# Performance work log

Hardware: AMD Instinct MI355X
Metric: run time of the kernel (lower is better)

Reference implementation:

```python
import jax, jax.numpy as jnp
import numpy as np

B, L, K, E, H, NH, W_OFF = 8, 512, 16, 32, 1, 64, 1
DK = E // H


def setup_inputs() -> dict:
    key = jax.random.key(0)
    ks = jax.random.split(key, 12)
    return {
        "time_steps": jax.random.uniform(ks[0], (B, L), jnp.float32),
        "val": jax.random.normal(ks[1], (B, L), jnp.float32),
        "mark": jax.random.randint(ks[2], (B, L), 1, K + 1, dtype=jnp.int32),
        "non_pad_mask": jnp.ones((B, L, 1), jnp.float32),
        "Wl": jax.random.normal(ks[3], (1, 1), jnp.float32) * 0.5,
        "bl": jnp.zeros((1,), jnp.float32),
        "Wp": jax.random.normal(ks[4], (E - 1, 1), jnp.float32) * 0.5,
        "bp": jnp.zeros((E - 1,), jnp.float32),
        "Wq": jax.random.normal(ks[5], (E, E), jnp.float32) / np.sqrt(E).astype(np.float32),
        "bq": jnp.zeros((E,), jnp.float32),
        "Wk": jax.random.normal(ks[6], (E, E), jnp.float32) / np.sqrt(E).astype(np.float32),
        "bk": jnp.zeros((E,), jnp.float32),
        "Wo": jax.random.normal(ks[7], (NH, K * H), jnp.float32) / np.sqrt(K * H).astype(np.float32),
        "bo": jnp.zeros((NH,), jnp.float32),
        "W_ih": jax.random.normal(ks[8], (3 * NH, NH), jnp.float32) / np.sqrt(NH).astype(np.float32),
        "W_hh": jax.random.normal(ks[9], (3 * NH, NH), jnp.float32) / np.sqrt(NH).astype(np.float32),
        "b_ih": jnp.zeros((3 * NH,), jnp.float32),
        "b_hh": jnp.zeros((3 * NH,), jnp.float32),
    }


def _forward(time_steps, val, mark, non_pad_mask,
             Wl, bl, Wp, bp, Wq, bq, Wk, bk, Wo, bo,
             W_ih, W_hh, b_ih, b_hh):
    # transform_to_3d_ts: scatter each (b,l) event into its channel mark-1
    npm = non_pad_mask[:, :, 0]                       # [B,L]
    onehot = (mark - 1)[:, :, None] == jnp.arange(K)[None, None, :]  # [B,L,K]
    valid = onehot & (npm > 0)[:, :, None]
    val_blk = jnp.where(valid, val[:, :, None], 0.0)          # [B,L,K]
    mask_blk = jnp.where(valid, npm[:, :, None], 0.0)         # [B,L,K]

    # learn_time_embedding
    tt = time_steps[:, :, None]                                # [B,L,1]
    key_emb = jnp.concatenate([tt @ Wl.T + bl, jnp.sin(tt @ Wp.T + bp)], axis=-1)  # [B,L,E]

    # subsequent mask (tril with diag offset w)
    att_mask = jnp.tril(jnp.ones((L, L), jnp.float32), W_OFF)  # [L,L]

    # multiTimeAttention (query == key == key_emb)
    q = (key_emb @ Wq.T + bq).reshape(B, L, H, DK).transpose(0, 2, 1, 3)  # [B,H,L,DK]
    k = (key_emb @ Wk.T + bk).reshape(B, L, H, DK).transpose(0, 2, 1, 3)
    scores = jnp.einsum('bhqd,bhkd->bhqk', q, k) / jnp.sqrt(jnp.float32(DK))  # [B,H,L,L]
    # broadcast to [B,H,L,L,K] (repeat_interleave equivalent), apply att_mask then pad mask
    scores5 = scores[..., None] * att_mask[None, None, :, :, None]
    scores5 = jnp.where(mask_blk[:, None, None, :, :] == 0, -1e9, scores5)
    p_attn = jax.nn.softmax(scores5, axis=-2)                  # softmax over key positions
    x = jnp.sum(p_attn * val_blk[:, None, None, :, :], axis=-2)  # [B,H,L,K]
    x = x.transpose(0, 2, 1, 3).reshape(B, L, H * K)
    att_out = x @ Wo.T + bo                                    # [B,L,NH]

    # single-layer GRU over time (PyTorch gate equations)
    def step(h, xt):
        gi = xt @ W_ih.T + b_ih
        gh = h @ W_hh.T + b_hh
        ir, iz, inn = jnp.split(gi, 3, axis=-1)
        hr, hz, hn = jnp.split(gh, 3, axis=-1)
        r = jax.nn.sigmoid(ir + hr)
        z = jax.nn.sigmoid(iz + hz)
        n = jnp.tanh(inn + r * hn)
        h_new = (1.0 - z) * n + z * h
        return h_new, h_new

    h0 = jnp.zeros((B, NH), att_out.dtype)
    _, outs = jax.lax.scan(step, h0, att_out.transpose(1, 0, 2))  # [L,B,NH]
    return outs.transpose(1, 0, 2)                                # [B,L,NH]


def reference(time_steps, val, mark, non_pad_mask,
              Wl, bl, Wp, bp, Wq, bq, Wk, bk, Wo, bo,
              W_ih, W_hh, b_ih, b_hh):
    return _forward(time_steps, val, mark, non_pad_mask,
                    Wl, bl, Wp, bp, Wq, bq, Wk, bk, Wo, bo,
                    W_ih, W_hh, b_ih, b_hh)
```

## Files before the change

kernel.cpp:

```cpp
#include <hip/hip_runtime.h>
#include <math.h>

#define B_    8
#define L_    512
#define K_    16
#define E_    32
#define NH_   64
#define WOFF_ 1


typedef float v2f __attribute__((ext_vector_type(2)));
typedef float v4f __attribute__((ext_vector_type(4)));

__global__ __launch_bounds__(256) void k_fused(
    const float* __restrict__ ts,   const float* __restrict__ val,
    const int*   __restrict__ mark, const float* __restrict__ npm,
    const float* __restrict__ Wl,   const float* __restrict__ bl,
    const float* __restrict__ Wp,   const float* __restrict__ bp,
    const float* __restrict__ Wq,   const float* __restrict__ bq,
    const float* __restrict__ Wk,   const float* __restrict__ bk,
    const float* __restrict__ Wo,   const float* __restrict__ bo,
    const float* __restrict__ Wih,  const float* __restrict__ bih,
    float* __restrict__ gi)
{
    __shared__ float kL[32 * 512];
    __shared__ float qL[16 * 32];
    __shared__ float srow[4 * 512];
    __shared__ int   cc[512];
    __shared__ float vv[512];
    __shared__ float attL[16 * 64];
    __shared__ float WqL[1024], WkL[1024];
    __shared__ float bqL[32], bkL[32], WpL[31], bpL[31];
    __shared__ float wl0, bl0;

    const int tid = threadIdx.x;
    const int qb  = blockIdx.x;
    const int b   = blockIdx.y;
    const int qb0 = qb * 16;

    {
        float4 v = ((const float4*)Wq)[tid];
        ((float4*)WqL)[tid] = v;
        float4 u = ((const float4*)Wk)[tid];
        ((float4*)WkL)[tid] = u;
    }
    if (tid < 32) { bqL[tid] = bq[tid]; bkL[tid] = bk[tid]; }
    if (tid < 31) { WpL[tid] = Wp[tid]; bpL[tid] = bp[tid]; }
    if (tid == 0) { wl0 = Wl[0]; bl0 = bl[0]; }
    for (int k = tid; k < 512; k += 256) {
        const int   m  = mark[b * 512 + k];
        const float np = npm[b * 512 + k];
        cc[k] = (np > 0.0f) ? (m - 1) : -1;
        vv[k] = val[b * 512 + k];
    }
    __syncthreads();

    for (int l = tid; l < 512; l += 256) {
        const float t = ts[b * 512 + l];
        float e[32];
        e[0] = t * wl0 + bl0;
        #pragma unroll
        for (int j = 1; j < 32; ++j) e[j] = sinf(t * WpL[j - 1] + bpL[j - 1]);

        const bool ownq = (l >= qb0) && (l < qb0 + 16);
        float* qrow = qL + (l - qb0) * 32;

        for (int dq = 0; dq < 8; ++dq) {
            float k0 = bkL[4*dq+0], k1 = bkL[4*dq+1], k2 = bkL[4*dq+2], k3 = bkL[4*dq+3];
            const float* wk = &WkL[(4*dq) * 32];
            #pragma unroll
            for (int j = 0; j < 32; ++j) {
                const float ej = e[j];
                k0 = fmaf(wk[j],      ej, k0);
                k1 = fmaf(wk[32 + j], ej, k1);
                k2 = fmaf(wk[64 + j], ej, k2);
                k3 = fmaf(wk[96 + j], ej, k3);
            }
            kL[(4*dq + 0) * 512 + l] = k0;
            kL[(4*dq + 1) * 512 + l] = k1;
            kL[(4*dq + 2) * 512 + l] = k2;
            kL[(4*dq + 3) * 512 + l] = k3;

            if (ownq) {
                float q0 = bqL[4*dq+0], q1 = bqL[4*dq+1], q2 = bqL[4*dq+2], q3 = bqL[4*dq+3];
                const float* wq = &WqL[(4*dq) * 32];
                #pragma unroll
                for (int j = 0; j < 32; ++j) {
                    const float ej = e[j];
                    q0 = fmaf(wq[j],      ej, q0);
                    q1 = fmaf(wq[32 + j], ej, q1);
                    q2 = fmaf(wq[64 + j], ej, q2);
                    q3 = fmaf(wq[96 + j], ej, q3);
                }
                qrow[4*dq + 0] = q0;
                qrow[4*dq + 1] = q1;
                qrow[4*dq + 2] = q2;
                qrow[4*dq + 3] = q3;
            }
        }
    }
    __syncthreads();

    const int w = tid >> 6, lane = tid & 63;

    for (int iq = 0; iq < 4; ++iq) {
        const int q = qb0 + w * 4 + iq;

        float qr[32];
        const float4* qm4 = (const float4*)(qL + (size_t)(q - qb0) * 32);
        #pragma unroll
        for (int j4 = 0; j4 < 8; ++j4) {
            float4 v = qm4[j4];
            qr[4*j4+0] = v.x; qr[4*j4+1] = v.y; qr[4*j4+2] = v.z; qr[4*j4+3] = v.w;
        }

        float acc[8];
        #pragma unroll
        for (int m = 0; m < 8; ++m) acc[m] = 0.0f;
        #pragma unroll 4
        for (int j = 0; j < 32; ++j) {
            const float* row = kL + j * 512 + lane;
            const float  qj  = qr[j];
            #pragma unroll
            for (int m = 0; m < 8; ++m) acc[m] = fmaf(qj, row[m * 64], acc[m]);
        }
        #pragma unroll
        for (int m = 0; m < 8; ++m)
            srow[w * 512 + m * 64 + lane] = acc[m] * 0.17677669529663687f;
        __syncthreads();

        const int c = lane & 15, s = lane >> 4;
        float mx = -1e30f, Z = 0.0f, X = 0.0f;
        const int base = s * 128;
        for (int t = 0; t < 128; ++t) {
            const int k = base + ((t + s) & 127);
            if (cc[k] == c) {
                const float l  = (k <= q + WOFF_) ? srow[w * 512 + k] : 0.0f;
                const float mn = fmaxf(mx, l);
                const float e1 = __expf(l - mn);
                const float sc = __expf(mx - mn);
                Z = Z * sc + e1;
                X = X * sc + e1 * vv[k];
                mx = mn;
            }
        }
        #pragma unroll
        for (int off = 16; off <= 32; off <<= 1) {
            const float mo = __shfl_xor(mx, off);
            const float Zo = __shfl_xor(Z, off);
            const float Xo = __shfl_xor(X, off);
            const float mn = fmaxf(mx, mo);
            const float a0 = __expf(mx - mn);
            const float a1 = __expf(mo - mn);
            Z = Z * a0 + Zo * a1;
            X = X * a0 + Xo * a1;
            mx = mn;
        }
        const float x = (Z > 0.0f) ? X / Z : 0.0f;

        float xs[16];
        #pragma unroll
        for (int c2 = 0; c2 < 16; ++c2) xs[c2] = __shfl(x, c2);

        const float4* wo4 = (const float4*)(Wo + lane * 16);
        float a = bo[lane];
        #pragma unroll
        for (int c4 = 0; c4 < 4; ++c4) {
            float4 v = wo4[c4];
            a += xs[4*c4+0] * v.x + xs[4*c4+1] * v.y + xs[4*c4+2] * v.z + xs[4*c4+3] * v.w;
        }
        attL[(w * 4 + iq) * 64 + lane] = a;
        __syncthreads();
    }

    const size_t out0 = (size_t)(b * 32 + qb) * 16 * 192;
    for (int pp = 0; pp < 12; ++pp) {
        const int p = tid + 256 * pp;
        const int r = p / 192, g = p - r * 192;
        float a0 = bih[g], a1 = 0.f, a2 = 0.f, a3 = 0.f;
        const float* wrow = Wih + g * 64;
        const float* arow = &attL[r * 64];
        #pragma unroll
        for (int j = 0; j < 64; j += 4) {
            a0 = fmaf(arow[j + 0], wrow[j + 0], a0);
            a1 = fmaf(arow[j + 1], wrow[j + 1], a1);
            a2 = fmaf(arow[j + 2], wrow[j + 2], a2);
            a3 = fmaf(arow[j + 3], wrow[j + 3], a3);
        }
        gi[out0 + p] = (a0 + a1) + (a2 + a3);
    }
}


#define GRU_STEP(u, DO_REFILL) {                                           \
    v4f hv[16];                                                            \
                                       \
    _Pragma("unroll")                                                      \
    for (int k = 0; k < 6; ++k) hv[k] = hs4[k];                            \
    const float gr = pr[u], gz = pz[u], gn = pn[u];                        \
    if (DO_REFILL) {                                                       \
        pr[u] = pf[0];                                                     \
        pz[u] = pf[64];                                                    \
        pn[u] = pf[128];                                                   \
        pf += 192;                                                         \
    }                                                                      \
    v2f ar2 = {gr + br, 0.0f};                                             \
    v2f az2 = {gz + bz, 0.0f};                                             \
    v2f an2 = {bn, 0.0f};                                                  \
    _Pragma("unroll")                                                      \
    for (int k = 0; k < 16; ++k) {                                         \
        if (k < 10) hv[k + 6] = hs4[k + 6];              \
        v2f p0 = __builtin_shufflevector(hv[k], hv[k], 0, 1);              \
        v2f p1 = __builtin_shufflevector(hv[k], hv[k], 2, 3);              \
        ar2 = wr[2*k]     * p0 + ar2;                    \
        az2 = wz[2*k]     * p0 + az2;                                      \
        an2 = wn[2*k]     * p0 + an2;                                      \
        ar2 = wr[2*k + 1] * p1 + ar2;                                      \
        az2 = wz[2*k + 1] * p1 + az2;                                      \
        an2 = wn[2*k + 1] * p1 + an2;                                      \
    }                                                                      \
    const float ar = ar2.x + ar2.y;                                        \
    const float az = az2.x + az2.y;                                        \
    const float hn = an2.x + an2.y;                                        \
    const float r = __builtin_amdgcn_rcpf(1.0f + __expf(-ar));             \
    const float z = __builtin_amdgcn_rcpf(1.0f + __expf(-az));             \
    float npre = gn + r * hn;                                              \
    npre = fminf(fmaxf(npre, -15.0f), 15.0f);                              \
    const float e2 = __expf(2.0f * npre);                                  \
    const float n  = (e2 - 1.0f) * __builtin_amdgcn_rcpf(e2 + 1.0f);       \
    h = fmaf(z, h - n, n);                              \
    hs[lane] = h;                        \
    *outp = h;                                        \
    outp += 64;                                                            \
}

__global__ __launch_bounds__(64, 1) void k_gru(
    const float* __restrict__ gi, const float* __restrict__ Whh,
    const float* __restrict__ bhh, float* __restrict__ out)
{
    __shared__ float hs[64];
    const int lane = threadIdx.x;
    const int b    = blockIdx.x;

    v2f wr[32], wz[32], wn[32];
    {
        const v2f* r2 = (const v2f*)(Whh + (size_t)lane * 64);
        const v2f* z2 = (const v2f*)(Whh + (size_t)(lane + 64) * 64);
        const v2f* n2 = (const v2f*)(Whh + (size_t)(lane + 128) * 64);
        #pragma unroll
        for (int j = 0; j < 32; ++j) {
            wr[j] = r2[j];
            wz[j] = z2[j];
            wn[j] = n2[j];
        }
    }
    const float br = bhh[lane];
    const float bz = bhh[lane + 64];
    const float bn = bhh[lane + 128];

    const float* gib  = gi  + (size_t)b * 512 * 192;
    float*       outp = out + (size_t)b * 512 * 64 + lane;

    float h = 0.0f;
    hs[lane] = 0.0f;

    float pr[2], pz[2], pn[2];
    #pragma unroll
    for (int i = 0; i < 2; ++i) {
        const float* gp = gib + (size_t)i * 192;
        pr[i] = gp[lane];
        pz[i] = gp[lane + 64];
        pn[i] = gp[lane + 128];
    }
    const float* pf = gib + (size_t)2 * 192 + lane;

    const v4f* hs4 = (const v4f*)hs;

    for (int tt = 0; tt < 510; tt += 2) {
        GRU_STEP(0, 1)
        GRU_STEP(1, 1)
    }
    GRU_STEP(0, 0)
    GRU_STEP(1, 0)
}

extern "C" void kernel_launch(void* const* d_in, const int* in_sizes, int n_in,
                              void* d_out, int out_size, void* d_ws, size_t ws_size,
                              hipStream_t stream)
{
    const float* ts   = (const float*)d_in[0];
    const float* val  = (const float*)d_in[1];
    const int*   mark = (const int*)  d_in[2];
    const float* npm  = (const float*)d_in[3];
    const float* Wl   = (const float*)d_in[4];
    const float* bl   = (const float*)d_in[5];
    const float* Wp   = (const float*)d_in[6];
    const float* bp   = (const float*)d_in[7];
    const float* Wq   = (const float*)d_in[8];
    const float* bq   = (const float*)d_in[9];
    const float* Wk   = (const float*)d_in[10];
    const float* bk   = (const float*)d_in[11];
    const float* Wo   = (const float*)d_in[12];
    const float* bo   = (const float*)d_in[13];
    const float* Wih  = (const float*)d_in[14];
    const float* Whh  = (const float*)d_in[15];
    const float* bih  = (const float*)d_in[16];
    const float* bhh  = (const float*)d_in[17];

    float* ws    = (float*)d_ws;
    float* gi    = ws + 524288;
    float* out   = (float*)d_out;

    k_fused<<<dim3(32, 8), 256, 0, stream>>>(ts, val, mark, npm, Wl, bl, Wp, bp,
                                             Wq, bq, Wk, bk, Wo, bo, Wih, bih, gi);
    k_gru<<<8, 64, 0, stream>>>(gi, Whh, bhh, out);
}
```

Measured before the change: 384.5 us.

## Fuse attention and GRU kernels with per-chunk flags to overlap the recurrence

Merges the attention/input-projection kernel and the GRU recurrence into one launch. The first 8 blocks run the GRU and spin on per-(batch, chunk) flags, and the remaining 256 blocks compute gi chunks and release a flag when each chunk is done. The GRU can then start on early time chunks while later ones are still being computed, hiding most of the attention phase and removing the second launch. It depends on all blocks being co-resident to avoid deadlock, and it adds a memset plus spin-waiting overhead.

```diff
diff --git a/kernel.cpp b/kernel.cpp
--- a/kernel.cpp
+++ b/kernel.cpp
@@ -12,7 +12,54 @@
 typedef float v2f __attribute__((ext_vector_type(2)));
 typedef float v4f __attribute__((ext_vector_type(4)));
 
-__global__ __launch_bounds__(256) void k_fused(
+
+#define GRU_STEP(u, DO_REFILL) {                                           \
+    v4f hv[16];                                                            \
+    _Pragma("unroll")                                                      \
+    for (int k = 0; k < 6; ++k) hv[k] = hs4[k];                            \
+    const float gr = pr[u], gz = pz[u], gn = pn[u];                        \
+    if (DO_REFILL) {                                                       \
+        pr[u] = pf[0];                                                     \
+        pz[u] = pf[64];                                                    \
+        pn[u] = pf[128];                                                   \
+        pf += 192;                                                         \
+    }                                                                      \
+    v2f ar2 = {gr + br, 0.0f};                                             \
+    v2f az2 = {gz + bz, 0.0f};                                             \
+    v2f an2 = {bn, 0.0f};                                                  \
+    _Pragma("unroll")                                                      \
+    for (int k = 0; k < 16; ++k) {                                         \
+        if (k < 10) hv[k + 6] = hs4[k + 6];                                \
+        v2f p0 = __builtin_shufflevector(hv[k], hv[k], 0, 1);              \
+        v2f p1 = __builtin_shufflevector(hv[k], hv[k], 2, 3);              \
+        ar2 = wr[2*k]     * p0 + ar2;                                      \
+        az2 = wz[2*k]     * p0 + az2;                                      \
+        an2 = wn[2*k]     * p0 + an2;                                      \
+        ar2 = wr[2*k + 1] * p1 + ar2;                                      \
+        az2 = wz[2*k + 1] * p1 + az2;                                      \
+        an2 = wn[2*k + 1] * p1 + an2;                                      \
+    }                                                                      \
+    const float ar = ar2.x + ar2.y;                                        \
+    const float az = az2.x + az2.y;                                        \
+    const float hn = an2.x + an2.y;                                        \
+    const float r = __builtin_amdgcn_rcpf(1.0f + __expf(-ar));             \
+    const float z = __builtin_amdgcn_rcpf(1.0f + __expf(-az));             \
+    float npre = gn + r * hn;                                              \
+    npre = fminf(fmaxf(npre, -15.0f), 15.0f);                              \
+    const float e2 = __expf(2.0f * npre);                                  \
+    const float n  = (e2 - 1.0f) * __builtin_amdgcn_rcpf(e2 + 1.0f);       \
+    h = fmaf(z, h - n, n);                                                 \
+    hsg[lane] = h;                                                         \
+    *outp = h;                                                             \
+    outp += 64;                                                            \
+}
+
+#define WAITFLAG(bb, cc)                                                   \
+    while (__hip_atomic_load(&flags[((bb) << 5) + (cc)],                   \
+           __ATOMIC_ACQUIRE, __HIP_MEMORY_SCOPE_AGENT) == 0)               \
+        __builtin_amdgcn_s_sleep(8);
+
+__global__ __launch_bounds__(256, 1) void k_mega(
     const float* __restrict__ ts,   const float* __restrict__ val,
     const int*   __restrict__ mark, const float* __restrict__ npm,
     const float* __restrict__ Wl,   const float* __restrict__ bl,
@@ -21,7 +68,9 @@
     const float* __restrict__ Wk,   const float* __restrict__ bk,
     const float* __restrict__ Wo,   const float* __restrict__ bo,
     const float* __restrict__ Wih,  const float* __restrict__ bih,
-    float* __restrict__ gi)
+    const float* __restrict__ Whh,  const float* __restrict__ bhh,
+    float* __restrict__ gi,         int* __restrict__ flags,
+    float* __restrict__ out)
 {
     __shared__ float kL[32 * 512];
     __shared__ float qL[16 * 32];
@@ -32,10 +81,73 @@
     __shared__ float WqL[1024], WkL[1024];
     __shared__ float bqL[32], bkL[32], WpL[31], bpL[31];
     __shared__ float wl0, bl0;
+    __shared__ float hsg[64];
 
     const int tid = threadIdx.x;
-    const int qb  = blockIdx.x;
-    const int b   = blockIdx.y;
+
+    if (blockIdx.x < 8) {
+        if (tid >= 64) return;
+        const int lane = tid;
+        const int b    = blockIdx.x;
+
+        v2f wr[32], wz[32], wn[32];
+        {
+            const v2f* r2 = (const v2f*)(Whh + (size_t)lane * 64);
+            const v2f* z2 = (const v2f*)(Whh + (size_t)(lane + 64) * 64);
+            const v2f* n2 = (const v2f*)(Whh + (size_t)(lane + 128) * 64);
+            #pragma unroll
+            for (int j = 0; j < 32; ++j) {
+                wr[j] = r2[j];
+                wz[j] = z2[j];
+                wn[j] = n2[j];
+            }
+        }
+        const float br = bhh[lane];
+        const float bz = bhh[lane + 64];
+        const float bn = bhh[lane + 128];
+
+        const float* gib  = gi  + (size_t)b * 512 * 192;
+        float*       outp = out + (size_t)b * 512 * 64 + lane;
+
+        float h = 0.0f;
+        hsg[lane] = 0.0f;
+
+        WAITFLAG(b, 0)
+
+        float pr[2], pz[2], pn[2];
+        #pragma unroll
+        for (int i = 0; i < 2; ++i) {
+            const float* gp = gib + (size_t)i * 192;
+            pr[i] = gp[lane];
+            pz[i] = gp[lane + 64];
+            pn[i] = gp[lane + 128];
+        }
+        const float* pf = gib + (size_t)2 * 192 + lane;
+
+        const v4f* hs4 = (const v4f*)hsg;
+
+        for (int c = 0; c < 32; ++c) {
+            if (c < 31) {
+                WAITFLAG(b, c + 1)
+                for (int g8 = 0; g8 < 8; ++g8) {
+                    GRU_STEP(0, 1)
+                    GRU_STEP(1, 1)
+                }
+            } else {
+                for (int g8 = 0; g8 < 7; ++g8) {
+                    GRU_STEP(0, 1)
+                    GRU_STEP(1, 1)
+                }
+                GRU_STEP(0, 0)
+                GRU_STEP(1, 0)
+            }
+        }
+        return;
+    }
+
+    const int pid = blockIdx.x - 8;
+    const int qb  = pid >> 3;
+    const int b   = pid & 7;
     const int qb0 = qb * 16;
 
     {
@@ -189,99 +301,13 @@
         }
         gi[out0 + p] = (a0 + a1) + (a2 + a3);
     }
-}
-
-
-#define GRU_STEP(u, DO_REFILL) {                                           \
-    v4f hv[16];                                                            \
-                                       \
-    _Pragma("unroll")                                                      \
-    for (int k = 0; k < 6; ++k) hv[k] = hs4[k];                            \
-    const float gr = pr[u], gz = pz[u], gn = pn[u];                        \
-    if (DO_REFILL) {                                                       \
-        pr[u] = pf[0];                                                     \
-        pz[u] = pf[64];                                                    \
-        pn[u] = pf[128];                                                   \
-        pf += 192;                                                         \
-    }                                                                      \
-    v2f ar2 = {gr + br, 0.0f};                                             \
-    v2f az2 = {gz + bz, 0.0f};                                             \
-    v2f an2 = {bn, 0.0f};                                                  \
-    _Pragma("unroll")                                                      \
-    for (int k = 0; k < 16; ++k) {                                         \
-        if (k < 10) hv[k + 6] = hs4[k + 6];              \
-        v2f p0 = __builtin_shufflevector(hv[k], hv[k], 0, 1);              \
-        v2f p1 = __builtin_shufflevector(hv[k], hv[k], 2, 3);              \
-        ar2 = wr[2*k]     * p0 + ar2;                    \
-        az2 = wz[2*k]     * p0 + az2;                                      \
-        an2 = wn[2*k]     * p0 + an2;                                      \
-        ar2 = wr[2*k + 1] * p1 + ar2;                                      \
-        az2 = wz[2*k + 1] * p1 + az2;                                      \
-        an2 = wn[2*k + 1] * p1 + an2;                                      \
-    }                                                                      \
-    const float ar = ar2.x + ar2.y;                                        \
-    const float az = az2.x + az2.y;                                        \
-    const float hn = an2.x + an2.y;                                        \
-    const float r = __builtin_amdgcn_rcpf(1.0f + __expf(-ar));             \
-    const float z = __builtin_amdgcn_rcpf(1.0f + __expf(-az));             \
-    float npre = gn + r * hn;                                              \
-    npre = fminf(fmaxf(npre, -15.0f), 15.0f);                              \
-    const float e2 = __expf(2.0f * npre);                                  \
-    const float n  = (e2 - 1.0f) * __builtin_amdgcn_rcpf(e2 + 1.0f);       \
-    h = fmaf(z, h - n, n);                              \
-    hs[lane] = h;                        \
-    *outp = h;                                        \
-    outp += 64;                                                            \
-}
-
-__global__ __launch_bounds__(64, 1) void k_gru(
-    const float* __restrict__ gi, const float* __restrict__ Whh,
-    const float* __restrict__ bhh, float* __restrict__ out)
-{
-    __shared__ float hs[64];
-    const int lane = threadIdx.x;
-    const int b    = blockIdx.x;
-
-    v2f wr[32], wz[32], wn[32];
-    {
-        const v2f* r2 = (const v2f*)(Whh + (size_t)lane * 64);
-        const v2f* z2 = (const v2f*)(Whh + (size_t)(lane + 64) * 64);
-        const v2f* n2 = (const v2f*)(Whh + (size_t)(lane + 128) * 64);
-        #pragma unroll
-        for (int j = 0; j < 32; ++j) {
-            wr[j] = r2[j];
-            wz[j] = z2[j];
-            wn[j] = n2[j];
-        }
-    }
-    const float br = bhh[lane];
-    const float bz = bhh[lane + 64];
-    const float bn = bhh[lane + 128];
-
-    const float* gib  = gi  + (size_t)b * 512 * 192;
-    float*       outp = out + (size_t)b * 512 * 64 + lane;
-
-    float h = 0.0f;
-    hs[lane] = 0.0f;
-
-    float pr[2], pz[2], pn[2];
-    #pragma unroll
-    for (int i = 0; i < 2; ++i) {
-        const float* gp = gib + (size_t)i * 192;
-        pr[i] = gp[lane];
-        pz[i] = gp[lane + 64];
-        pn[i] = gp[lane + 128];
-    }
-    const float* pf = gib + (size_t)2 * 192 + lane;
-
-    const v4f* hs4 = (const v4f*)hs;
-
-    for (int tt = 0; tt < 510; tt += 2) {
-        GRU_STEP(0, 1)
-        GRU_STEP(1, 1)
-    }
-    GRU_STEP(0, 0)
-    GRU_STEP(1, 0)
+
+    __syncthreads();
+    if (tid == 0) {
+        __threadfence();
+        __hip_atomic_store(&flags[(b << 5) + qb], 1,
+                           __ATOMIC_RELEASE, __HIP_MEMORY_SCOPE_AGENT);
+    }
 }
 
 extern "C" void kernel_launch(void* const* d_in, const int* in_sizes, int n_in,
@@ -308,10 +334,12 @@
     const float* bhh  = (const float*)d_in[17];
 
     float* ws    = (float*)d_ws;
+    int*   flags = (int*)d_ws;
     float* gi    = ws + 524288;
     float* out   = (float*)d_out;
 
-    k_fused<<<dim3(32, 8), 256, 0, stream>>>(ts, val, mark, npm, Wl, bl, Wp, bp,
-                                             Wq, bq, Wk, bk, Wo, bo, Wih, bih, gi);
-    k_gru<<<8, 64, 0, stream>>>(gi, Whh, bhh, out);
+    hipMemsetAsync(flags, 0, 256 * sizeof(int), stream);
+    k_mega<<<264, 256, 0, stream>>>(ts, val, mark, npm, Wl, bl, Wp, bp,
+                                    Wq, bq, Wk, bk, Wo, bo, Wih, bih,
+                                    Whh, bhh, gi, flags, out);
 }
```

Measured after the change: 421.3 us. +9.6%, slower.
